# Kernel tuning notes

Hardware: AMD Instinct MI355X
Metric: run time of the kernel (lower is better)

## Reference

```python
import jax, jax.numpy as jnp
import numpy as np

K = 5  # kernel_size
PAD = K // 2


def _median_filter(x):
    # x: [B,1,H,W]; reflect pad then 5x5 window median (lower median of 25 elems == true median)
    B, C, H, W = x.shape
    xp = jnp.pad(x, ((0, 0), (0, 0), (PAD, PAD), (PAD, PAD)), mode='reflect')
    windows = jnp.stack([xp[:, :, dy:dy + H, dx:dx + W]
                         for dy in range(K) for dx in range(K)], axis=0)
    return jnp.median(windows, axis=0)


def _gaussian_kernel(sigma):
    c = K // 2
    coords = jnp.arange(K, dtype=jnp.float32) - c
    d2 = coords[:, None] ** 2 + coords[None, :] ** 2  # [K,K]
    kern = jnp.exp(-d2 / (2.0 * sigma ** 2)) / (2.0 * jnp.pi * sigma ** 2)
    kern = kern / kern.sum()
    return kern[None, None]  # [1,1,K,K] (OIHW, single channel, groups=1)


def setup_inputs() -> dict:
    key = jax.random.key(0)
    img = jax.random.normal(key, (8, 1024, 1024), dtype=jnp.float32)
    sigma = jnp.float32(4.0)  # learnable parameter of the Gaussian filter
    return {"img": img, "sigma": sigma}


def reference(img, sigma):
    x = img[:, None]           # [B,1,H,W]
    x = _median_filter(x)      # [B,1,H,W]
    kern = _gaussian_kernel(sigma)
    x = jax.lax.conv_general_dilated(
        x, kern, window_strides=(1, 1),
        padding=[(PAD, PAD), (PAD, PAD)],
        dimension_numbers=('NCHW', 'OIHW', 'NCHW'))
    return x[:, 0]             # [B,H,W]
```

## Files before the change

kernel.cpp:

```cpp
#include <hip/hip_runtime.h>

#define HH 1024
#define WW 1024
#define NIMG 8
#define TROWS 16
#define NSTEP (TROWS + 4)

__device__ __forceinline__ float med3f(float a, float b, float c) {
    return __builtin_amdgcn_fmed3f(a, b, c);
}
__device__ __forceinline__ float min3f(float a, float b, float c) {
    return fminf(fminf(a, b), c);
}
__device__ __forceinline__ float max3f(float a, float b, float c) {
    return fmaxf(fmaxf(a, b), c);
}

__device__ __forceinline__ void sort5(float& a, float& b, float& c, float& d, float& e) {
    float l3 = min3f(a, b, c);
    float m3 = med3f(a, b, c);
    float h3 = max3f(a, b, c);
    float s0 = fminf(l3, d);
    float s1 = med3f(l3, m3, d);
    float s2 = med3f(m3, h3, d);
    float s3 = fmaxf(h3, d);
    float r0 = fminf(s0, e);
    float r1 = med3f(s0, s1, e);
    float r2 = med3f(s1, s2, e);
    float r3 = med3f(s2, s3, e);
    float r4 = fmaxf(s3, e);
    a = r0; b = r1; c = r2; d = r3; e = r4;
}
__device__ __forceinline__ void top2(float a, float b, float c, float d, float e,
                                     float& r3, float& r4) {
    float m3 = med3f(a, b, c);
    float h3 = max3f(a, b, c);
    float s2 = med3f(m3, h3, d);
    float s3 = fmaxf(h3, d);
    r3 = med3f(s2, s3, e);
    r4 = fmaxf(s3, e);
}
__device__ __forceinline__ void bot2(float a, float b, float c, float d, float e,
                                     float& r0, float& r1) {
    float l3 = min3f(a, b, c);
    float m3 = med3f(a, b, c);
    float s0 = fminf(l3, d);
    float s1 = med3f(l3, m3, d);
    r0 = fminf(s0, e);
    r1 = med3f(s0, s1, e);
}
__device__ __forceinline__ void top3(float a, float b, float c, float d, float e,
                                     float& r2, float& r3, float& r4) {
    float l3 = min3f(a, b, c);
    float m3 = med3f(a, b, c);
    float h3 = max3f(a, b, c);
    float s1 = med3f(l3, m3, d);
    float s2 = med3f(m3, h3, d);
    float s3 = fmaxf(h3, d);
    r2 = med3f(s1, s2, e);
    r3 = med3f(s2, s3, e);
    r4 = fmaxf(s3, e);
}
__device__ __forceinline__ void bot3(float a, float b, float c, float d, float e,
                                     float& r0, float& r1, float& r2) {
    float l3 = min3f(a, b, c);
    float m3 = med3f(a, b, c);
    float h3 = max3f(a, b, c);
    float s0 = fminf(l3, d);
    float s1 = med3f(l3, m3, d);
    float s2 = med3f(m3, h3, d);
    r0 = fminf(s0, e);
    r1 = med3f(s0, s1, e);
    r2 = med3f(s1, s2, e);
}
__device__ __forceinline__ void mid3(float a, float b, float c, float d, float e,
                                     float& r1, float& r2, float& r3) {
    float l3 = min3f(a, b, c);
    float m3 = med3f(a, b, c);
    float h3 = max3f(a, b, c);
    float s0 = fminf(l3, d);
    float s1 = med3f(l3, m3, d);
    float s2 = med3f(m3, h3, d);
    float s3 = fmaxf(h3, d);
    r1 = med3f(s0, s1, e);
    r2 = med3f(s1, s2, e);
    r3 = med3f(s2, s3, e);
}

__device__ __forceinline__ void loadrow(const float* __restrict__ base, int r,
                                        int tid, int x0, float (&d)[8]) {
    const int rr = (r < 0) ? -r : (r >= HH ? 2 * HH - 2 - r : r);
    const float* rp = base + (size_t)rr * WW;
    const float4 A = *reinterpret_cast<const float4*>(rp + (tid == 0   ? x0 : x0 - 4));
    const float4 B = *reinterpret_cast<const float4*>(rp + x0);
    const float4 C = *reinterpret_cast<const float4*>(rp + (tid == 255 ? x0 : x0 + 4));
    d[0] = (tid == 0)   ? B.z : A.z;
    d[1] = (tid == 0)   ? B.y : A.w;
    d[2] = B.x; d[3] = B.y; d[4] = B.z; d[5] = B.w;
    d[6] = (tid == 255) ? B.z : C.x;
    d[7] = (tid == 255) ? B.y : C.y;
}

template<int P>
__device__ __forceinline__ void median4(const float (&ring)[6][8], float (&med)[4]) {
    float S0[8], S1[8], S2[8], S3[8], S4[8];
    #pragma unroll
    for (int c = 0; c < 8; ++c) {
        float a = ring[P % 6][c];
        float b = ring[(P + 1) % 6][c];
        float g = ring[(P + 2) % 6][c];
        float d = ring[(P + 3) % 6][c];
        float e = ring[(P + 4) % 6][c];
        sort5(a, b, g, d, e);
        S0[c] = a; S1[c] = b; S2[c] = g; S3[c] = d; S4[c] = e;
    }
    #pragma unroll
    for (int j = 0; j < 4; ++j) {
        float r03, r04, r12, r13, r14, r21, r22, r23, r30, r31, r32, r40, r41;
        top2(S0[j], S0[j+1], S0[j+2], S0[j+3], S0[j+4], r03, r04);
        top3(S1[j], S1[j+1], S1[j+2], S1[j+3], S1[j+4], r12, r13, r14);
        mid3(S2[j], S2[j+1], S2[j+2], S2[j+3], S2[j+4], r21, r22, r23);
        bot3(S3[j], S3[j+1], S3[j+2], S3[j+3], S3[j+4], r30, r31, r32);
        bot2(S4[j], S4[j+1], S4[j+2], S4[j+3], S4[j+4], r40, r41);
        float u = fminf(r40, r31), v = fmaxf(r40, r31);
        float w = fminf(v, r32),  x = fmaxf(v, r32);
        float ps0 = r30, ps1 = u, ps2 = w;
        float ps3 = fminf(x, r41), ps4 = fmaxf(x, r41);
        float q0 = fminf(r21, r03);
        float q1 = med3f(r21, r22, r03);
        float q2 = med3f(r22, r23, r03);
        float t1 = fminf(q1, r04);
        float t2 = med3f(q1, q2, r04);
        float t3 = med3f(q2, r23, r04);
        float t4 = fmaxf(r23, r04);
        float Y0 = fmaxf(ps0, q0);
        float Y1 = fmaxf(ps1, t1);
        float X2 = fminf(ps2, t2), Y2 = fmaxf(ps2, t2);
        float X3 = fminf(ps3, t3);
        float X4 = fminf(ps4, t4);
        float L  = max3f(X2, Y0, r12);
        float M  = med3f(X3, Y1, r13);
        float Hc = min3f(X4, Y2, r14);
        med[j] = med3f(L, M, Hc);
    }
}

template<int P>
__device__ __forceinline__ void step(int s, int y0, int tid, int x0,
                                     const float* __restrict__ base,
                                     float* __restrict__ obase,
                                     const float (&wv)[5],
                                     float (&ring)[6][8], float (&hr)[6][4],
                                     float (*lbuf)[1040]) {
    float hh[8];
    if (s >= 1) {
        const float* Lb = lbuf[(s + 1) & 1];
        const float4 Ha = *reinterpret_cast<const float4*>(&Lb[x0]);
        const float4 Hb = *reinterpret_cast<const float4*>(&Lb[x0 + 4]);
        hh[0] = Ha.x; hh[1] = Ha.y; hh[2] = Ha.z; hh[3] = Ha.w;
        hh[4] = Hb.x; hh[5] = Hb.y; hh[6] = Hb.z; hh[7] = Hb.w;
    }
    if (s < NSTEP - 1) loadrow(base, y0 + s + 1, tid, x0, ring[(P + 5) % 6]);

    float med[4] = {0.f, 0.f, 0.f, 0.f};
    const int m = y0 - 2 + s;
    if (s < NSTEP && m >= 0 && m < HH) median4<P>(ring, med);

    if (s < NSTEP) {
        float* Lw = lbuf[s & 1];
        *reinterpret_cast<float2*>(&Lw[x0 + 2]) = make_float2(med[0], med[1]);
        *reinterpret_cast<float2*>(&Lw[x0 + 4]) = make_float2(med[2], med[3]);
    }

    if (s >= 1) {
        #pragma unroll
        for (int j = 0; j < 4; ++j) {
            float h = 0.f;
            #pragma unroll
            for (int c = 0; c < 5; ++c) h = fmaf(wv[c], hh[j + c], h);
            hr[(P + 5) % 6][j] = h;
        }
    }

    if (s >= 5) {
        const int o = y0 + s - 5;
        float a0 = 0.f, a1 = 0.f, a2 = 0.f, a3 = 0.f;
        #pragma unroll
        for (int k = 0; k < 5; ++k) {
            const int   sl = (P + 1 + k) % 6;
            const float wy = wv[k];
            a0 = fmaf(wy, hr[sl][0], a0);
            a1 = fmaf(wy, hr[sl][1], a1);
            a2 = fmaf(wy, hr[sl][2], a2);
            a3 = fmaf(wy, hr[sl][3], a3);
        }
        *reinterpret_cast<float4*>(obase + (size_t)o * WW + x0) =
            make_float4(a0, a1, a2, a3);
    }
    __syncthreads();
}

__global__ __launch_bounds__(256, 2) void fused_kernel(const float* __restrict__ in,
                                                       const float* __restrict__ sig,
                                                       float* __restrict__ out) {
    const int bi   = blockIdx.x;
    const int img  = bi & 7;
    const int tile = bi >> 3;
    const int y0   = tile * TROWS;
    const int tid  = threadIdx.x;
    const int x0   = tid * 4;
    const float* base  = in  + (size_t)img * HH * WW;
    float*       obase = out + (size_t)img * HH * WW;

    const float sigma  = sig[0];
    const float inv2s2 = 1.0f / (2.0f * sigma * sigma);
    const float g1 = expf(-1.0f * inv2s2);
    const float g4 = expf(-4.0f * inv2s2);
    const float sn = 1.0f + 2.0f * g1 + 2.0f * g4;
    const float wv[5] = { g4 / sn, g1 / sn, 1.0f / sn, g1 / sn, g4 / sn };

    __shared__ float lbuf[2][1040];
    if (tid < 2) {
        lbuf[tid][0] = 0.f; lbuf[tid][1] = 0.f;
        lbuf[tid][1026] = 0.f; lbuf[tid][1027] = 0.f;
    }

    float ring[6][8];
    float hr[6][4];

    #pragma unroll
    for (int k = 0; k < 5; ++k) loadrow(base, y0 - 4 + k, tid, x0, ring[k]);

    for (int outer = 0; outer < 3; ++outer) {
        const int sb = outer * 6;
        step<0>(sb + 0, y0, tid, x0, base, obase, wv, ring, hr, lbuf);
        step<1>(sb + 1, y0, tid, x0, base, obase, wv, ring, hr, lbuf);
        step<2>(sb + 2, y0, tid, x0, base, obase, wv, ring, hr, lbuf);
        step<3>(sb + 3, y0, tid, x0, base, obase, wv, ring, hr, lbuf);
        step<4>(sb + 4, y0, tid, x0, base, obase, wv, ring, hr, lbuf);
        step<5>(sb + 5, y0, tid, x0, base, obase, wv, ring, hr, lbuf);
    }
    step<0>(18, y0, tid, x0, base, obase, wv, ring, hr, lbuf);
    step<1>(19, y0, tid, x0, base, obase, wv, ring, hr, lbuf);
    step<2>(20, y0, tid, x0, base, obase, wv, ring, hr, lbuf);
}

extern "C" void kernel_launch(void* const* d_in, const int* in_sizes, int n_in,
                              void* d_out, int out_size, void* d_ws, size_t ws_size,
                              hipStream_t stream) {
    const float* img = (const float*)d_in[0];
    const float* sig = (const float*)d_in[1];
    float* out = (float*)d_out;

    dim3 grid(NIMG * (HH / TROWS));
    dim3 block(256);
    hipLaunchKernelGGL(fused_kernel, grid, block, 0, stream, img, sig, out);
}
```

Baseline: 39.22 us.

## Process two median rows per step sharing a 4-row column sort

Each step now produces two output median rows at once. It sorts the four shared middle rows of each column once and then merges in the fifth row separately for the top window and the bottom window, which cuts the vertical sorting work. The tile height is halved to 8 rows, the number of barriers per tile drops, and the launch bounds ask for 4 blocks per CU instead of 2. The costs are a larger register ring of 8 rows, twice as many shared-memory buffers, and a larger relative halo overhead (4 extra rows per 8 output rows instead of per 16).

Result: slower. 97.87 us (+149.5%).

```diff
diff --git a/kernel.cpp b/kernel.cpp
--- a/kernel.cpp
+++ b/kernel.cpp
@@ -3,8 +3,7 @@
 #define HH 1024
 #define WW 1024
 #define NIMG 8
-#define TROWS 16
-#define NSTEP (TROWS + 4)
+#define TROWS 8
 
 __device__ __forceinline__ float med3f(float a, float b, float c) {
     return __builtin_amdgcn_fmed3f(a, b, c);
@@ -16,21 +15,6 @@
     return fmaxf(fmaxf(a, b), c);
 }
 
-__device__ __forceinline__ void sort5(float& a, float& b, float& c, float& d, float& e) {
-    float l3 = min3f(a, b, c);
-    float m3 = med3f(a, b, c);
-    float h3 = max3f(a, b, c);
-    float s0 = fminf(l3, d);
-    float s1 = med3f(l3, m3, d);
-    float s2 = med3f(m3, h3, d);
-    float s3 = fmaxf(h3, d);
-    float r0 = fminf(s0, e);
-    float r1 = med3f(s0, s1, e);
-    float r2 = med3f(s1, s2, e);
-    float r3 = med3f(s2, s3, e);
-    float r4 = fmaxf(s3, e);
-    a = r0; b = r1; c = r2; d = r3; e = r4;
-}
 __device__ __forceinline__ void top2(float a, float b, float c, float d, float e,
                                      float& r3, float& r4) {
     float m3 = med3f(a, b, c);
@@ -101,19 +85,9 @@
     d[7] = (tid == 255) ? B.y : C.y;
 }
 
-template<int P>
-__device__ __forceinline__ void median4(const float (&ring)[6][8], float (&med)[4]) {
-    float S0[8], S1[8], S2[8], S3[8], S4[8];
-    #pragma unroll
-    for (int c = 0; c < 8; ++c) {
-        float a = ring[P % 6][c];
-        float b = ring[(P + 1) % 6][c];
-        float g = ring[(P + 2) % 6][c];
-        float d = ring[(P + 3) % 6][c];
-        float e = ring[(P + 4) % 6][c];
-        sort5(a, b, g, d, e);
-        S0[c] = a; S1[c] = b; S2[c] = g; S3[c] = d; S4[c] = e;
-    }
+__device__ __forceinline__ void med4net(const float (&S0)[8], const float (&S1)[8],
+                                        const float (&S2)[8], const float (&S3)[8],
+                                        const float (&S4)[8], float (&med)[4]) {
     #pragma unroll
     for (int j = 0; j < 4; ++j) {
         float r03, r04, r12, r13, r14, r21, r22, r23, r30, r31, r32, r40, r41;
@@ -145,62 +119,136 @@
     }
 }
 
-template<int P>
-__device__ __forceinline__ void step(int s, int y0, int tid, int x0,
-                                     const float* __restrict__ base,
-                                     float* __restrict__ obase,
-                                     const float (&wv)[5],
-                                     float (&ring)[6][8], float (&hr)[6][4],
-                                     float (*lbuf)[1040]) {
-    float hh[8];
-    if (s >= 1) {
-        const float* Lb = lbuf[(s + 1) & 1];
-        const float4 Ha = *reinterpret_cast<const float4*>(&Lb[x0]);
-        const float4 Hb = *reinterpret_cast<const float4*>(&Lb[x0 + 4]);
-        hh[0] = Ha.x; hh[1] = Ha.y; hh[2] = Ha.z; hh[3] = Ha.w;
-        hh[4] = Hb.x; hh[5] = Hb.y; hh[6] = Hb.z; hh[7] = Hb.w;
-    }
-    if (s < NSTEP - 1) loadrow(base, y0 + s + 1, tid, x0, ring[(P + 5) % 6]);
-
-    float med[4] = {0.f, 0.f, 0.f, 0.f};
-    const int m = y0 - 2 + s;
-    if (s < NSTEP && m >= 0 && m < HH) median4<P>(ring, med);
-
-    if (s < NSTEP) {
-        float* Lw = lbuf[s & 1];
-        *reinterpret_cast<float2*>(&Lw[x0 + 2]) = make_float2(med[0], med[1]);
-        *reinterpret_cast<float2*>(&Lw[x0 + 4]) = make_float2(med[2], med[3]);
-    }
-
-    if (s >= 1) {
+template<int K>
+__device__ __forceinline__ void dstep(int y0, int tid, int x0,
+                                      const float* __restrict__ base,
+                                      float* __restrict__ obase,
+                                      const float (&wv)[5],
+                                      float (&ring)[8][8], float (&hr)[6][4],
+                                      float (*lbuf)[1032]) {
+    float ha[8], hb[8];
+    if constexpr (K >= 1) {
+        const float* La = lbuf[2 * ((K + 1) & 1)];
+        const float* Lb = lbuf[2 * ((K + 1) & 1) + 1];
+        const float4 a0 = *reinterpret_cast<const float4*>(&La[x0]);
+        const float4 a1 = *reinterpret_cast<const float4*>(&La[x0 + 4]);
+        const float4 b0 = *reinterpret_cast<const float4*>(&Lb[x0]);
+        const float4 b1 = *reinterpret_cast<const float4*>(&Lb[x0 + 4]);
+        ha[0]=a0.x; ha[1]=a0.y; ha[2]=a0.z; ha[3]=a0.w;
+        ha[4]=a1.x; ha[5]=a1.y; ha[6]=a1.z; ha[7]=a1.w;
+        hb[0]=b0.x; hb[1]=b0.y; hb[2]=b0.z; hb[3]=b0.w;
+        hb[4]=b1.x; hb[5]=b1.y; hb[6]=b1.z; hb[7]=b1.w;
+    }
+    if constexpr (K <= 4) {
+        loadrow(base, y0 + 2 + 2 * K, tid, x0, ring[(2 * K + 6) & 7]);
+        loadrow(base, y0 + 3 + 2 * K, tid, x0, ring[(2 * K + 7) & 7]);
+    }
+    if constexpr (K <= 5) {
+        constexpr int s0 = (2*K) & 7,     s1 = (2*K + 1) & 7, s2 = (2*K + 2) & 7;
+        constexpr int s3 = (2*K + 3) & 7, s4 = (2*K + 4) & 7, s5 = (2*K + 5) & 7;
+        float T0[8], T1[8], T2[8], T3[8];
+        #pragma unroll
+        for (int c = 0; c < 8; ++c) {
+            float b = ring[s1][c], cc = ring[s2][c], d = ring[s3][c], e = ring[s4][c];
+            float l3 = min3f(b, cc, d);
+            float m3 = med3f(b, cc, d);
+            float h3 = max3f(b, cc, d);
+            T0[c] = fminf(l3, e);
+            T1[c] = med3f(l3, m3, e);
+            T2[c] = med3f(m3, h3, e);
+            T3[c] = fmaxf(h3, e);
+        }
+        const int m0 = y0 - 2 + 2 * K;
+        float med0[4] = {0.f, 0.f, 0.f, 0.f};
+        float med1[4] = {0.f, 0.f, 0.f, 0.f};
+        if (m0 >= 0 && m0 < HH) {
+            float S0[8], S1[8], S2[8], S3[8], S4[8];
+            #pragma unroll
+            for (int c = 0; c < 8; ++c) {
+                float a = ring[s0][c];
+                S0[c] = fminf(T0[c], a);
+                S1[c] = med3f(T0[c], T1[c], a);
+                S2[c] = med3f(T1[c], T2[c], a);
+                S3[c] = med3f(T2[c], T3[c], a);
+                S4[c] = fmaxf(T3[c], a);
+            }
+            med4net(S0, S1, S2, S3, S4, med0);
+        }
+        const int m1 = m0 + 1;
+        if (m1 >= 0 && m1 < HH) {
+            float S0[8], S1[8], S2[8], S3[8], S4[8];
+            #pragma unroll
+            for (int c = 0; c < 8; ++c) {
+                float f = ring[s5][c];
+                S0[c] = fminf(T0[c], f);
+                S1[c] = med3f(T0[c], T1[c], f);
+                S2[c] = med3f(T1[c], T2[c], f);
+                S3[c] = med3f(T2[c], T3[c], f);
+                S4[c] = fmaxf(T3[c], f);
+            }
+            med4net(S0, S1, S2, S3, S4, med1);
+        }
+        float* Lw0 = lbuf[2 * (K & 1)];
+        float* Lw1 = lbuf[2 * (K & 1) + 1];
+        *reinterpret_cast<float2*>(&Lw0[x0 + 2]) = make_float2(med0[0], med0[1]);
+        *reinterpret_cast<float2*>(&Lw0[x0 + 4]) = make_float2(med0[2], med0[3]);
+        *reinterpret_cast<float2*>(&Lw1[x0 + 2]) = make_float2(med1[0], med1[1]);
+        *reinterpret_cast<float2*>(&Lw1[x0 + 4]) = make_float2(med1[2], med1[3]);
+    }
+    if constexpr (K >= 1) {
         #pragma unroll
         for (int j = 0; j < 4; ++j) {
             float h = 0.f;
             #pragma unroll
-            for (int c = 0; c < 5; ++c) h = fmaf(wv[c], hh[j + c], h);
-            hr[(P + 5) % 6][j] = h;
-        }
-    }
-
-    if (s >= 5) {
-        const int o = y0 + s - 5;
-        float a0 = 0.f, a1 = 0.f, a2 = 0.f, a3 = 0.f;
+            for (int c = 0; c < 5; ++c) h = fmaf(wv[c], ha[j + c], h);
+            hr[(2 * K) % 6][j] = h;
+        }
         #pragma unroll
-        for (int k = 0; k < 5; ++k) {
-            const int   sl = (P + 1 + k) % 6;
-            const float wy = wv[k];
-            a0 = fmaf(wy, hr[sl][0], a0);
-            a1 = fmaf(wy, hr[sl][1], a1);
-            a2 = fmaf(wy, hr[sl][2], a2);
-            a3 = fmaf(wy, hr[sl][3], a3);
-        }
-        *reinterpret_cast<float4*>(obase + (size_t)o * WW + x0) =
-            make_float4(a0, a1, a2, a3);
-    }
-    __syncthreads();
-}
-
-__global__ __launch_bounds__(256, 2) void fused_kernel(const float* __restrict__ in,
+        for (int j = 0; j < 4; ++j) {
+            float h = 0.f;
+            #pragma unroll
+            for (int c = 0; c < 5; ++c) h = fmaf(wv[c], hb[j + c], h);
+            hr[(2 * K + 1) % 6][j] = h;
+        }
+    }
+    if constexpr (K >= 3) {
+        {
+            const int o0 = y0 - 6 + 2 * K;
+            float a0 = 0.f, a1 = 0.f, a2 = 0.f, a3 = 0.f;
+            #pragma unroll
+            for (int k = 0; k < 5; ++k) {
+                constexpr int base_sl = 2 * K - 4;
+                const int   sl = (base_sl + k) % 6;
+                const float wy = wv[k];
+                a0 = fmaf(wy, hr[sl][0], a0);
+                a1 = fmaf(wy, hr[sl][1], a1);
+                a2 = fmaf(wy, hr[sl][2], a2);
+                a3 = fmaf(wy, hr[sl][3], a3);
+            }
+            *reinterpret_cast<float4*>(obase + (size_t)o0 * WW + x0) =
+                make_float4(a0, a1, a2, a3);
+        }
+        {
+            const int o1 = y0 - 5 + 2 * K;
+            float a0 = 0.f, a1 = 0.f, a2 = 0.f, a3 = 0.f;
+            #pragma unroll
+            for (int k = 0; k < 5; ++k) {
+                constexpr int base_sl = 2 * K - 3;
+                const int   sl = (base_sl + k) % 6;
+                const float wy = wv[k];
+                a0 = fmaf(wy, hr[sl][0], a0);
+                a1 = fmaf(wy, hr[sl][1], a1);
+                a2 = fmaf(wy, hr[sl][2], a2);
+                a3 = fmaf(wy, hr[sl][3], a3);
+            }
+            *reinterpret_cast<float4*>(obase + (size_t)o1 * WW + x0) =
+                make_float4(a0, a1, a2, a3);
+        }
+    }
+    if constexpr (K < 6) __syncthreads();
+}
+
+__global__ __launch_bounds__(256, 4) void fused_kernel(const float* __restrict__ in,
                                                        const float* __restrict__ sig,
                                                        float* __restrict__ out) {
     const int bi   = blockIdx.x;
@@ -219,30 +267,26 @@
     const float sn = 1.0f + 2.0f * g1 + 2.0f * g4;
     const float wv[5] = { g4 / sn, g1 / sn, 1.0f / sn, g1 / sn, g4 / sn };
 
-    __shared__ float lbuf[2][1040];
-    if (tid < 2) {
-        lbuf[tid][0] = 0.f; lbuf[tid][1] = 0.f;
-        lbuf[tid][1026] = 0.f; lbuf[tid][1027] = 0.f;
-    }
-
-    float ring[6][8];
+    __shared__ float lbuf[4][1032];
+    if (tid < 8) {
+        const int r = tid >> 1, p = tid & 1;
+        lbuf[r][p] = 0.f;
+        lbuf[r][1026 + p] = 0.f;
+    }
+
+    float ring[8][8];
     float hr[6][4];
 
     #pragma unroll
-    for (int k = 0; k < 5; ++k) loadrow(base, y0 - 4 + k, tid, x0, ring[k]);
-
-    for (int outer = 0; outer < 3; ++outer) {
-        const int sb = outer * 6;
-        step<0>(sb + 0, y0, tid, x0, base, obase, wv, ring, hr, lbuf);
-        step<1>(sb + 1, y0, tid, x0, base, obase, wv, ring, hr, lbuf);
-        step<2>(sb + 2, y0, tid, x0, base, obase, wv, ring, hr, lbuf);
-        step<3>(sb + 3, y0, tid, x0, base, obase, wv, ring, hr, lbuf);
-        step<4>(sb + 4, y0, tid, x0, base, obase, wv, ring, hr, lbuf);
-        step<5>(sb + 5, y0, tid, x0, base, obase, wv, ring, hr, lbuf);
-    }
-    step<0>(18, y0, tid, x0, base, obase, wv, ring, hr, lbuf);
-    step<1>(19, y0, tid, x0, base, obase, wv, ring, hr, lbuf);
-    step<2>(20, y0, tid, x0, base, obase, wv, ring, hr, lbuf);
+    for (int k = 0; k < 6; ++k) loadrow(base, y0 - 4 + k, tid, x0, ring[k]);
+
+    dstep<0>(y0, tid, x0, base, obase, wv, ring, hr, lbuf);
+    dstep<1>(y0, tid, x0, base, obase, wv, ring, hr, lbuf);
+    dstep<2>(y0, tid, x0, base, obase, wv, ring, hr, lbuf);
+    dstep<3>(y0, tid, x0, base, obase, wv, ring, hr, lbuf);
+    dstep<4>(y0, tid, x0, base, obase, wv, ring, hr, lbuf);
+    dstep<5>(y0, tid, x0, base, obase, wv, ring, hr, lbuf);
+    dstep<6>(y0, tid, x0, base, obase, wv, ring, hr, lbuf);
 }
 
 extern "C" void kernel_launch(void* const* d_in, const int* in_sizes, int n_in,
```
